# Kernel optimization log

Measured on AMD Instinct MI355X. Metric: run time of the kernel, lower is better.

## Reference

```python
import jax, jax.numpy as jnp
import numpy as np

N_DIM = 768
HIDDEN_DIM = 768
BATCH = 4
SEQ = 2048


def setup_inputs() -> dict:
    key = jax.random.key(0)
    ks = jax.random.split(key, 9)
    s_in = 1.0 / np.sqrt(N_DIM)
    s_h = 1.0 / np.sqrt(HIDDEN_DIM)
    return {
        "x": jax.random.normal(ks[0], (BATCH, SEQ, N_DIM), dtype=jnp.float32),
        # torch Linear weights: [out_features, in_features]
        "wq": jax.random.uniform(ks[1], (HIDDEN_DIM, N_DIM), jnp.float32, -s_in, s_in),
        "bq": jax.random.uniform(ks[2], (HIDDEN_DIM,), jnp.float32, -s_in, s_in),
        "wk": jax.random.uniform(ks[3], (HIDDEN_DIM, N_DIM), jnp.float32, -s_in, s_in),
        "bk": jax.random.uniform(ks[4], (HIDDEN_DIM,), jnp.float32, -s_in, s_in),
        "wv": jax.random.uniform(ks[5], (HIDDEN_DIM, N_DIM), jnp.float32, -s_in, s_in),
        "bv": jax.random.uniform(ks[6], (HIDDEN_DIM,), jnp.float32, -s_in, s_in),
        "wo": jax.random.uniform(ks[7], (N_DIM, HIDDEN_DIM), jnp.float32, -s_h, s_h),
        "bo": jax.random.uniform(ks[8], (N_DIM,), jnp.float32, -s_h, s_h),
    }


def reference(x, wq, bq, wk, bk, wv, bv, wo, bo):
    # q,k,v: [B, S, H]
    q = jnp.einsum("bsd,hd->bsh", x, wq) + bq
    k = jnp.einsum("bsd,hd->bsh", x, wk) + bk
    v = jnp.einsum("bsd,hd->bsh", x, wv) + bv
    # NOTE: faithful to source — no 1/sqrt(d) scaling, no mask.
    scores = jnp.einsum("bqh,bkh->bqk", q, k)  # [B, S, S]
    attn = jax.nn.softmax(scores, axis=-1)
    y = jnp.einsum("bqk,bkh->bqh", attn, v)  # [B, S, H]
    out = jnp.einsum("bsh,dh->bsd", y, wo) + bo
    return out
```

## Files before the change

kernel.cpp:

```cpp
#include <hip/hip_runtime.h>

typedef _Float16 f16;
typedef _Float16 f16x8 __attribute__((ext_vector_type(8)));
typedef float f32x4 __attribute__((ext_vector_type(4)));

#define GLD16(g, l) __builtin_amdgcn_global_load_lds( \
    (const __attribute__((address_space(1))) void*)(g), \
    (__attribute__((address_space(3))) void*)(l), 16, 0, 0)

template <typename OutT, int BM, int BN, int MODE, int MINW>
__global__ __launch_bounds__(256, MINW)
void gemm_kernel(const f16* __restrict__ A, long sA,
                 const f16* __restrict__ B, long sB,
                 void* __restrict__ Cv, long sC,
                 void* __restrict__ C2v,
                 const float* __restrict__ bias,
                 const float* __restrict__ bias2,
                 int N, int K)
{
    constexpr int FM = BM / 32;
    constexpr int FN = BN / 32;
    constexpr int IA = BM / 32;
    constexpr int IB = BN / 32;

    OutT* C  = (OutT*)Cv;
    OutT* C2 = (OutT*)C2v;
    const int tid  = threadIdx.x;
    const int wave = tid >> 6;
    const int lane = tid & 63;
    const int bz   = blockIdx.z;
    A += (long)bz * sA;
    B += (long)bz * sB;
    C += (long)bz * sC;
    const long bm = (long)blockIdx.x * BM;
    const long bn = (long)blockIdx.y * BN;

    __shared__ f16 sAt[BM * 64];
    __shared__ f16 sBt[BN * 64];

    const int srow = lane >> 3;
    const int gch  = ((lane & 7) ^ srow) * 8;

    const f16* gAb = A + (bm + wave * (BM / 4) + srow) * (long)K + gch;
    const f16* gBb = B + (bn + wave * (BN / 4) + srow) * (long)K + gch;

    const int wm = (wave >> 1) * (BM / 2);
    const int wn = (wave & 1) * (BN / 2);
    const int lr = lane & 15;
    const int qd = lane >> 4;
    const int swz0 = ((0 * 4 + qd) ^ (lr & 7)) * 8;
    const int swz1 = ((1 * 4 + qd) ^ (lr & 7)) * 8;

    f32x4 acc[FM][FN] = {};

    for (int k0 = 0; k0 < K; k0 += 64) {
        #pragma unroll
        for (int i = 0; i < IA; ++i)
            GLD16(gAb + k0 + (long)i * 8 * K, &sAt[(wave * (BM / 4) + i * 8) * 64]);
        #pragma unroll
        for (int i = 0; i < IB; ++i)
            GLD16(gBb + k0 + (long)i * 8 * K, &sBt[(wave * (BN / 4) + i * 8) * 64]);
        __syncthreads();

        #pragma unroll
        for (int h = 0; h < 2; ++h) {
            const int swz = h ? swz1 : swz0;
            f16x8 af[FM], bf[FN];
            #pragma unroll
            for (int t = 0; t < FM; ++t)
                af[t] = *(const f16x8*)&sAt[(wm + t * 16 + lr) * 64 + swz];
            #pragma unroll
            for (int t = 0; t < FN; ++t)
                bf[t] = *(const f16x8*)&sBt[(wn + t * 16 + lr) * 64 + swz];
            #pragma unroll
            for (int tm = 0; tm < FM; ++tm)
                #pragma unroll
                for (int tn = 0; tn < FN; ++tn)
                    acc[tm][tn] = __builtin_amdgcn_mfma_f32_16x16x32_f16(
                        af[tm], bf[tn], acc[tm][tn], 0, 0, 0);
        }
        __syncthreads();
    }

    #pragma unroll
    for (int tn = 0; tn < FN; ++tn) {
        const long col = bn + wn + tn * 16 + lr;
        OutT* dst = C;
        long cc = col, stride = N;
        float bc = 0.f;
        if (MODE == 1) bc = bias[col];
        if (MODE == 3) {
            stride = 768;
            if (col >= 768) { dst = C2; cc = col - 768; bc = bias2[cc]; }
            else            { bc = bias[cc]; }
        }
        #pragma unroll
        for (int tm = 0; tm < FM; ++tm) {
            #pragma unroll
            for (int r = 0; r < 4; ++r) {
                const long row = bm + wm + tm * 16 + qd * 4 + r;
                float v = acc[tm][tn][r] + bc;
                if (MODE == 2) v += bias[row];
                dst[row * stride + cc] = (OutT)v;
            }
        }
    }
}

template <typename OutT, int BM, int BN, int MODE, int MINW>
__global__ __launch_bounds__(256, MINW)
void gemm_pipe4(const f16* __restrict__ A, long sA,
                const f16* __restrict__ B, long sB,
                void* __restrict__ Cv, long sC,
                void* __restrict__ C2v,
                const float* __restrict__ bias,
                const float* __restrict__ bias2,
                int N, int K)
{
    constexpr int FM = BM / 32;
    constexpr int FN = BN / 32;
    constexpr int IA = BM / 32;
    constexpr int IB = BN / 32;

    OutT* C  = (OutT*)Cv;
    OutT* C2 = (OutT*)C2v;
    const int tid  = threadIdx.x;
    const int wave = tid >> 6;
    const int lane = tid & 63;
    const int bz   = blockIdx.z;
    A += (long)bz * sA;
    B += (long)bz * sB;
    C += (long)bz * sC;
    const long bm = (long)blockIdx.x * BM;
    const long bn = (long)blockIdx.y * BN;

    __shared__ f16 sAt[2][BM * 64];
    __shared__ f16 sBt[2][BN * 64];

    const int srow = lane >> 3;
    const int gch  = ((lane & 7) ^ srow) * 8;

    const f16* gAb = A + (bm + wave * (BM / 4) + srow) * (long)K + gch;
    const f16* gBb = B + (bn + wave * (BN / 4) + srow) * (long)K + gch;

    const int wm = (wave >> 1) * (BM / 2);
    const int wn = (wave & 1) * (BN / 2);
    const int lr = lane & 15;
    const int qd = lane >> 4;
    const int swz0 = ((0 * 4 + qd) ^ (lr & 7)) * 8;
    const int swz1 = ((1 * 4 + qd) ^ (lr & 7)) * 8;

    f32x4 acc[FM][FN] = {};

    #pragma unroll
    for (int i = 0; i < IA; ++i)
        GLD16(gAb + (long)i * 8 * K, &sAt[0][(wave * (BM / 4) + i * 8) * 64]);
    #pragma unroll
    for (int i = 0; i < IB; ++i)
        GLD16(gBb + (long)i * 8 * K, &sBt[0][(wave * (BN / 4) + i * 8) * 64]);

    const int nt = K / 64;
    for (int t = 0; t < nt; ++t) {
        const int cur = t & 1;
        if (t + 1 < nt) {
            const long off = (long)(t + 1) * 64;
            #pragma unroll
            for (int i = 0; i < IA; ++i)
                GLD16(gAb + off + (long)i * 8 * K, &sAt[cur ^ 1][(wave * (BM / 4) + i * 8) * 64]);
            #pragma unroll
            for (int i = 0; i < IB; ++i)
                GLD16(gBb + off + (long)i * 8 * K, &sBt[cur ^ 1][(wave * (BN / 4) + i * 8) * 64]);
            asm volatile("s_waitcnt vmcnt(%0)" :: "n"(IA + IB));
        } else {
            asm volatile("s_waitcnt vmcnt(0)");
        }
        __builtin_amdgcn_s_barrier();

        #pragma unroll
        for (int h = 0; h < 2; ++h) {
            const int swz = h ? swz1 : swz0;
            f16x8 af[FM], bf[FN];
            #pragma unroll
            for (int t2 = 0; t2 < FM; ++t2)
                af[t2] = *(const f16x8*)&sAt[cur][(wm + t2 * 16 + lr) * 64 + swz];
            #pragma unroll
            for (int t2 = 0; t2 < FN; ++t2)
                bf[t2] = *(const f16x8*)&sBt[cur][(wn + t2 * 16 + lr) * 64 + swz];
            __builtin_amdgcn_s_setprio(1);
            #pragma unroll
            for (int tm = 0; tm < FM; ++tm)
                #pragma unroll
                for (int tn = 0; tn < FN; ++tn)
                    acc[tm][tn] = __builtin_amdgcn_mfma_f32_16x16x32_f16(
                        af[tm], bf[tn], acc[tm][tn], 0, 0, 0);
            __builtin_amdgcn_s_setprio(0);
        }
        __builtin_amdgcn_s_barrier();
    }

    #pragma unroll
    for (int tn = 0; tn < FN; ++tn) {
        const long col = bn + wn + tn * 16 + lr;
        OutT* dst = C;
        long cc = col, stride = N;
        float bc = 0.f;
        if (MODE == 1) bc = bias[col];
        if (MODE == 3) {
            stride = 768;
            if (col >= 768) { dst = C2; cc = col - 768; bc = bias2[cc]; }
            else            { bc = bias[cc]; }
        }
        #pragma unroll
        for (int tm = 0; tm < FM; ++tm) {
            #pragma unroll
            for (int r = 0; r < 4; ++r) {
                const long row = bm + wm + tm * 16 + qd * 4 + r;
                float v = acc[tm][tn][r] + bc;
                if (MODE == 2) v += bias[row];
                dst[row * stride + cc] = (OutT)v;
            }
        }
    }
}

__global__ __launch_bounds__(512, 2)
void gemm_pipe(const f16* __restrict__ A, long sA,
               const f16* __restrict__ B, long sB,
               f16* __restrict__ C, long sC,
               int N, int K)
{
    const int tid  = threadIdx.x;
    const int wave = tid >> 6;
    const int lane = tid & 63;
    const int bz   = blockIdx.z;
    A += (long)bz * sA;
    B += (long)bz * sB;
    C += (long)bz * sC;
    const long bm = (long)blockIdx.x * 256;
    const long bn = (long)blockIdx.y * 256;

    __shared__ f16 sAt[2][256 * 64];
    __shared__ f16 sBt[2][256 * 64];

    const int srow = lane >> 3;
    const int gch  = ((lane & 7) ^ srow) * 8;
    const f16* gA = A + (bm + wave * 32 + srow) * (long)K + gch;
    const f16* gB = B + (bn + wave * 32 + srow) * (long)K + gch;

    const int wm = (wave >> 2) * 128;
    const int wn = (wave & 3) * 64;
    const int lr = lane & 15;
    const int qd = lane >> 4;
    const int swz0 = ((0 * 4 + qd) ^ (lr & 7)) * 8;
    const int swz1 = ((1 * 4 + qd) ^ (lr & 7)) * 8;

    f32x4 acc[8][4] = {};

    #pragma unroll
    for (int i = 0; i < 4; ++i)
        GLD16(gA + (long)i * 8 * K, &sAt[0][(wave * 32 + i * 8) * 64]);
    #pragma unroll
    for (int i = 0; i < 4; ++i)
        GLD16(gB + (long)i * 8 * K, &sBt[0][(wave * 32 + i * 8) * 64]);

    const int nt = K / 64;
    for (int t = 0; t < nt; ++t) {
        const int cur = t & 1;
        if (t + 1 < nt) {
            const long off = (long)(t + 1) * 64;
            #pragma unroll
            for (int i = 0; i < 4; ++i)
                GLD16(gA + off + (long)i * 8 * K, &sAt[cur ^ 1][(wave * 32 + i * 8) * 64]);
            #pragma unroll
            for (int i = 0; i < 4; ++i)
                GLD16(gB + off + (long)i * 8 * K, &sBt[cur ^ 1][(wave * 32 + i * 8) * 64]);
            asm volatile("s_waitcnt vmcnt(8)");
        } else {
            asm volatile("s_waitcnt vmcnt(0)");
        }
        __builtin_amdgcn_s_barrier();

        #pragma unroll
        for (int h = 0; h < 2; ++h) {
            const int swz = h ? swz1 : swz0;
            f16x8 bf[4];
            #pragma unroll
            for (int c = 0; c < 4; ++c)
                bf[c] = *(const f16x8*)&sBt[cur][(wn + c * 16 + lr) * 64 + swz];
            #pragma unroll
            for (int rh = 0; rh < 2; ++rh) {
                f16x8 af[4];
                #pragma unroll
                for (int m = 0; m < 4; ++m)
                    af[m] = *(const f16x8*)&sAt[cur][(wm + rh * 64 + m * 16 + lr) * 64 + swz];
                __builtin_amdgcn_s_setprio(1);
                #pragma unroll
                for (int m = 0; m < 4; ++m)
                    #pragma unroll
                    for (int c = 0; c < 4; ++c)
                        acc[rh * 4 + m][c] = __builtin_amdgcn_mfma_f32_16x16x32_f16(
                            af[m], bf[c], acc[rh * 4 + m][c], 0, 0, 0);
                __builtin_amdgcn_s_setprio(0);
            }
        }
        __builtin_amdgcn_s_barrier();
    }

    #pragma unroll
    for (int cf = 0; cf < 4; ++cf) {
        const long col = bn + wn + cf * 16 + lr;
        #pragma unroll
        for (int rf = 0; rf < 8; ++rf) {
            #pragma unroll
            for (int r = 0; r < 4; ++r) {
                const long row = bm + wm + rf * 16 + qd * 4 + r;
                C[row * (long)N + col] = (f16)acc[rf][cf][r];
            }
        }
    }
}

__global__ __launch_bounds__(256)
void softmax_kernel(f16* __restrict__ S)
{
    const long row = blockIdx.x;
    f16* p = S + row * 2048;
    const int tid  = threadIdx.x;
    const int wave = tid >> 6;
    const int lane = tid & 63;

    f16x8 x = *(const f16x8*)&p[tid * 8];
    float v[8];
    float m = -1e30f;
    #pragma unroll
    for (int j = 0; j < 8; ++j) { v[j] = (float)x[j]; m = fmaxf(m, v[j]); }
    #pragma unroll
    for (int off = 32; off > 0; off >>= 1) m = fmaxf(m, __shfl_down(m, off));

    __shared__ float rm[4], rs[4];
    if (lane == 0) rm[wave] = m;
    __syncthreads();
    m = fmaxf(fmaxf(rm[0], rm[1]), fmaxf(rm[2], rm[3]));

    float s = 0.f;
    #pragma unroll
    for (int j = 0; j < 8; ++j) { v[j] = __expf(v[j] - m); s += v[j]; }
    #pragma unroll
    for (int off = 32; off > 0; off >>= 1) s += __shfl_down(s, off);
    if (lane == 0) rs[wave] = s;
    __syncthreads();
    s = rs[0] + rs[1] + rs[2] + rs[3];
    const float inv = 1.0f / s;

    f16x8 y;
    #pragma unroll
    for (int j = 0; j < 8; ++j) y[j] = (f16)(v[j] * inv);
    *(f16x8*)&p[tid * 8] = y;
}

__global__ __launch_bounds__(256)
void cvt_all_kernel(const float* __restrict__ x,
                    const float* __restrict__ w0, const float* __restrict__ w1,
                    const float* __restrict__ w2, const float* __restrict__ w3,
                    f16* __restrict__ x16, f16* __restrict__ w16)
{
    const float* in; f16* out; long i;
    if (blockIdx.x < 3072) {
        in = x; out = x16;
        i = ((long)blockIdx.x * 256 + threadIdx.x) * 8;
    } else {
        const int wb  = blockIdx.x - 3072;
        const int sel = wb / 288;
        in  = (sel == 0) ? w0 : (sel == 1) ? w1 : (sel == 2) ? w2 : w3;
        out = w16 + (long)sel * 589824;
        i = ((long)(wb - sel * 288) * 256 + threadIdx.x) * 8;
    }
    float4 a = *(const float4*)(in + i);
    float4 b = *(const float4*)(in + i + 4);
    f16x8 o;
    o[0] = (f16)a.x; o[1] = (f16)a.y; o[2] = (f16)a.z; o[3] = (f16)a.w;
    o[4] = (f16)b.x; o[5] = (f16)b.y; o[6] = (f16)b.z; o[7] = (f16)b.w;
    *(f16x8*)&out[i] = o;
}

extern "C" void kernel_launch(void* const* d_in, const int* in_sizes, int n_in,
                              void* d_out, int out_size, void* d_ws, size_t ws_size,
                              hipStream_t stream)
{
    const float* x  = (const float*)d_in[0];
    const float* wq = (const float*)d_in[1];
    const float* bq = (const float*)d_in[2];
    const float* wk = (const float*)d_in[3];
    const float* bk = (const float*)d_in[4];
    const float* wv = (const float*)d_in[5];
    const float* bv = (const float*)d_in[6];
    const float* wo = (const float*)d_in[7];
    const float* bo = (const float*)d_in[8];

    char* ws = (char*)d_ws;
    f16* x16 = (f16*)(ws + 0);
    f16* w16 = (f16*)(ws + 12582912);
    f16* Q   = (f16*)(ws + 17301504);
    f16* Kb  = (f16*)(ws + 29884416);
    f16* VT  = (f16*)(ws + 42467328);
    f16* S   = (f16*)(ws + 55050240);
    f16* Y   = (f16*)(ws + 88604672);

    f16* wv16 = w16 + 2 * 589824;
    f16* wo16 = w16 + 3 * 589824;

    cvt_all_kernel<<<4224, 256, 0, stream>>>(x, wq, wk, wv, wo, x16, w16);

    gemm_kernel<f16, 128, 128, 3, 3><<<dim3(64, 12, 1), 256, 0, stream>>>(
        x16, 0, w16, 0, Q, 0, Kb, bq, bk, 1536, 768);
    gemm_pipe4<f16, 64, 128, 2, 4><<<dim3(12, 16, 4), 256, 0, stream>>>(
        wv16, 0, x16, (long)2048 * 768, VT, (long)768 * 2048, nullptr,
        bv, nullptr, 2048, 768);
    gemm_pipe<<<dim3(8, 8, 4), 512, 0, stream>>>(
        Q, (long)2048 * 768, Kb, (long)2048 * 768, S, (long)2048 * 2048,
        2048, 768);
    softmax_kernel<<<8192, 256, 0, stream>>>(S);
    gemm_pipe4<f16, 128, 64, 0, 4><<<dim3(16, 12, 4), 256, 0, stream>>>(
        S, (long)2048 * 2048, VT, (long)768 * 2048, Y, (long)2048 * 768,
        nullptr, nullptr, nullptr, 768, 2048);
    gemm_pipe4<float, 128, 64, 1, 4><<<dim3(64, 12, 1), 256, 0, stream>>>(
        Y, 0, wo16, 0, (float*)d_out, 0, nullptr, bo, nullptr, 768, 768);
}
```

Before: 230.2 us.

## Replace double-buffered K=64 GEMM pipelines with 4-stage K=32 ring buffers

The two pipelined GEMM kernels move from a two-slot LDS double buffer with 64-wide K tiles to a four-slot ring of 32-wide K tiles. Three tiles are prefetched ahead, and each iteration uses a single barrier, so global-to-LDS loads get more latency slack. The LDS swizzle is redone for the narrower 32-element rows. In exchange there are twice as many iterations and barriers, and each barrier round carries less MFMA work.

```diff
diff --git a/kernel.cpp b/kernel.cpp
--- a/kernel.cpp
+++ b/kernel.cpp
@@ -7,6 +7,10 @@
 #define GLD16(g, l) __builtin_amdgcn_global_load_lds( \
     (const __attribute__((address_space(1))) void*)(g), \
     (__attribute__((address_space(3))) void*)(l), 16, 0, 0)
+
+#define WAITV(n) asm volatile("s_waitcnt vmcnt(%0)" :: "n"(n) : "memory")
+#define BAR() do { __builtin_amdgcn_s_barrier(); \
+                   __builtin_amdgcn_sched_barrier(0); } while (0)
 
 template <typename OutT, int BM, int BN, int MODE, int MINW>
 __global__ __launch_bounds__(256, MINW)
@@ -109,7 +113,7 @@
 
 template <typename OutT, int BM, int BN, int MODE, int MINW>
 __global__ __launch_bounds__(256, MINW)
-void gemm_pipe4(const f16* __restrict__ A, long sA,
+void gemm_ring4(const f16* __restrict__ A, long sA,
                 const f16* __restrict__ B, long sB,
                 void* __restrict__ Cv, long sC,
                 void* __restrict__ C2v,
@@ -119,8 +123,9 @@
 {
     constexpr int FM = BM / 32;
     constexpr int FN = BN / 32;
-    constexpr int IA = BM / 32;
-    constexpr int IB = BN / 32;
+    constexpr int IA = BM / 64;
+    constexpr int IB = BN / 64;
+    constexpr int L  = IA + IB;
 
     OutT* C  = (OutT*)Cv;
     OutT* C2 = (OutT*)C2v;
@@ -134,11 +139,11 @@
     const long bm = (long)blockIdx.x * BM;
     const long bn = (long)blockIdx.y * BN;
 
-    __shared__ f16 sAt[2][BM * 64];
-    __shared__ f16 sBt[2][BN * 64];
-
-    const int srow = lane >> 3;
-    const int gch  = ((lane & 7) ^ srow) * 8;
+    __shared__ f16 shA[4][BM * 32];
+    __shared__ f16 shB[4][BN * 32];
+
+    const int srow = lane >> 2;
+    const int gch  = ((lane & 3) ^ ((lane >> 3) & 3)) * 8;
 
     const f16* gAb = A + (bm + wave * (BM / 4) + srow) * (long)K + gch;
     const f16* gBb = B + (bn + wave * (BN / 4) + srow) * (long)K + gch;
@@ -147,56 +152,52 @@
     const int wn = (wave & 1) * (BN / 2);
     const int lr = lane & 15;
     const int qd = lane >> 4;
-    const int swz0 = ((0 * 4 + qd) ^ (lr & 7)) * 8;
-    const int swz1 = ((1 * 4 + qd) ^ (lr & 7)) * 8;
+    const int rdo = (qd ^ ((lr >> 1) & 3)) * 8;
 
     f32x4 acc[FM][FN] = {};
 
-    #pragma unroll
-    for (int i = 0; i < IA; ++i)
-        GLD16(gAb + (long)i * 8 * K, &sAt[0][(wave * (BM / 4) + i * 8) * 64]);
-    #pragma unroll
-    for (int i = 0; i < IB; ++i)
-        GLD16(gBb + (long)i * 8 * K, &sBt[0][(wave * (BN / 4) + i * 8) * 64]);
-
-    const int nt = K / 64;
-    for (int t = 0; t < nt; ++t) {
-        const int cur = t & 1;
-        if (t + 1 < nt) {
-            const long off = (long)(t + 1) * 64;
-            #pragma unroll
-            for (int i = 0; i < IA; ++i)
-                GLD16(gAb + off + (long)i * 8 * K, &sAt[cur ^ 1][(wave * (BM / 4) + i * 8) * 64]);
-            #pragma unroll
-            for (int i = 0; i < IB; ++i)
-                GLD16(gBb + off + (long)i * 8 * K, &sBt[cur ^ 1][(wave * (BN / 4) + i * 8) * 64]);
-            asm volatile("s_waitcnt vmcnt(%0)" :: "n"(IA + IB));
-        } else {
-            asm volatile("s_waitcnt vmcnt(0)");
-        }
-        __builtin_amdgcn_s_barrier();
-
-        #pragma unroll
-        for (int h = 0; h < 2; ++h) {
-            const int swz = h ? swz1 : swz0;
-            f16x8 af[FM], bf[FN];
-            #pragma unroll
-            for (int t2 = 0; t2 < FM; ++t2)
-                af[t2] = *(const f16x8*)&sAt[cur][(wm + t2 * 16 + lr) * 64 + swz];
-            #pragma unroll
-            for (int t2 = 0; t2 < FN; ++t2)
-                bf[t2] = *(const f16x8*)&sBt[cur][(wn + t2 * 16 + lr) * 64 + swz];
-            __builtin_amdgcn_s_setprio(1);
-            #pragma unroll
-            for (int tm = 0; tm < FM; ++tm)
-                #pragma unroll
-                for (int tn = 0; tn < FN; ++tn)
-                    acc[tm][tn] = __builtin_amdgcn_mfma_f32_16x16x32_f16(
-                        af[tm], bf[tn], acc[tm][tn], 0, 0, 0);
-            __builtin_amdgcn_s_setprio(0);
-        }
-        __builtin_amdgcn_s_barrier();
-    }
+    auto issue = [&](int tt) {
+        const int s = tt & 3;
+        const long ko = (long)tt * 32;
+        #pragma unroll
+        for (int i = 0; i < IA; ++i)
+            GLD16(gAb + ko + (long)i * 16 * K, &shA[s][(wave * (BM / 4) + i * 16) * 32]);
+        #pragma unroll
+        for (int i = 0; i < IB; ++i)
+            GLD16(gBb + ko + (long)i * 16 * K, &shB[s][(wave * (BN / 4) + i * 16) * 32]);
+    };
+
+    auto comp = [&](int tt) {
+        const int cur = tt & 3;
+        f16x8 af[FM], bf[FN];
+        #pragma unroll
+        for (int m = 0; m < FM; ++m)
+            af[m] = *(const f16x8*)&shA[cur][(wm + m * 16 + lr) * 32 + rdo];
+        #pragma unroll
+        for (int n = 0; n < FN; ++n)
+            bf[n] = *(const f16x8*)&shB[cur][(wn + n * 16 + lr) * 32 + rdo];
+        __builtin_amdgcn_s_setprio(1);
+        #pragma unroll
+        for (int m = 0; m < FM; ++m)
+            #pragma unroll
+            for (int n = 0; n < FN; ++n)
+                acc[m][n] = __builtin_amdgcn_mfma_f32_16x16x32_f16(
+                    af[m], bf[n], acc[m][n], 0, 0, 0);
+        __builtin_amdgcn_s_setprio(0);
+    };
+
+    const int nt = K / 32;
+    issue(0); issue(1); issue(2);
+
+    for (int t = 0; t < nt - 3; ++t) {
+        WAITV(2 * L);
+        BAR();
+        issue(t + 3);
+        comp(t);
+    }
+    WAITV(2 * L); BAR(); comp(nt - 3);
+    WAITV(L);     BAR(); comp(nt - 2);
+    WAITV(0);     BAR(); comp(nt - 1);
 
     #pragma unroll
     for (int tn = 0; tn < FN; ++tn) {
@@ -224,11 +225,12 @@
 }
 
 __global__ __launch_bounds__(512, 2)
-void gemm_pipe(const f16* __restrict__ A, long sA,
-               const f16* __restrict__ B, long sB,
-               f16* __restrict__ C, long sC,
-               int N, int K)
-{
+void gemm_ring8(const f16* __restrict__ A, long sA,
+                const f16* __restrict__ B, long sB,
+                f16* __restrict__ C, long sC,
+                int N, int K)
+{
+    constexpr int L = 4;
     const int tid  = threadIdx.x;
     const int wave = tid >> 6;
     const int lane = tid & 63;
@@ -239,11 +241,11 @@
     const long bm = (long)blockIdx.x * 256;
     const long bn = (long)blockIdx.y * 256;
 
-    __shared__ f16 sAt[2][256 * 64];
-    __shared__ f16 sBt[2][256 * 64];
-
-    const int srow = lane >> 3;
-    const int gch  = ((lane & 7) ^ srow) * 8;
+    __shared__ f16 shA[4][256 * 32];
+    __shared__ f16 shB[4][256 * 32];
+
+    const int srow = lane >> 2;
+    const int gch  = ((lane & 3) ^ ((lane >> 3) & 3)) * 8;
     const f16* gA = A + (bm + wave * 32 + srow) * (long)K + gch;
     const f16* gB = B + (bn + wave * 32 + srow) * (long)K + gch;
 
@@ -251,60 +253,56 @@
     const int wn = (wave & 3) * 64;
     const int lr = lane & 15;
     const int qd = lane >> 4;
-    const int swz0 = ((0 * 4 + qd) ^ (lr & 7)) * 8;
-    const int swz1 = ((1 * 4 + qd) ^ (lr & 7)) * 8;
+    const int rdo = (qd ^ ((lr >> 1) & 3)) * 8;
 
     f32x4 acc[8][4] = {};
 
-    #pragma unroll
-    for (int i = 0; i < 4; ++i)
-        GLD16(gA + (long)i * 8 * K, &sAt[0][(wave * 32 + i * 8) * 64]);
-    #pragma unroll
-    for (int i = 0; i < 4; ++i)
-        GLD16(gB + (long)i * 8 * K, &sBt[0][(wave * 32 + i * 8) * 64]);
-
-    const int nt = K / 64;
-    for (int t = 0; t < nt; ++t) {
-        const int cur = t & 1;
-        if (t + 1 < nt) {
-            const long off = (long)(t + 1) * 64;
-            #pragma unroll
-            for (int i = 0; i < 4; ++i)
-                GLD16(gA + off + (long)i * 8 * K, &sAt[cur ^ 1][(wave * 32 + i * 8) * 64]);
-            #pragma unroll
-            for (int i = 0; i < 4; ++i)
-                GLD16(gB + off + (long)i * 8 * K, &sBt[cur ^ 1][(wave * 32 + i * 8) * 64]);
-            asm volatile("s_waitcnt vmcnt(8)");
-        } else {
-            asm volatile("s_waitcnt vmcnt(0)");
-        }
-        __builtin_amdgcn_s_barrier();
-
-        #pragma unroll
-        for (int h = 0; h < 2; ++h) {
-            const int swz = h ? swz1 : swz0;
-            f16x8 bf[4];
-            #pragma unroll
-            for (int c = 0; c < 4; ++c)
-                bf[c] = *(const f16x8*)&sBt[cur][(wn + c * 16 + lr) * 64 + swz];
-            #pragma unroll
-            for (int rh = 0; rh < 2; ++rh) {
-                f16x8 af[4];
+    auto issue = [&](int tt) {
+        const int s = tt & 3;
+        const long ko = (long)tt * 32;
+        #pragma unroll
+        for (int i = 0; i < 2; ++i)
+            GLD16(gA + ko + (long)i * 16 * K, &shA[s][(wave * 32 + i * 16) * 32]);
+        #pragma unroll
+        for (int i = 0; i < 2; ++i)
+            GLD16(gB + ko + (long)i * 16 * K, &shB[s][(wave * 32 + i * 16) * 32]);
+    };
+
+    auto comp = [&](int tt) {
+        const int cur = tt & 3;
+        f16x8 bf[4];
+        #pragma unroll
+        for (int n = 0; n < 4; ++n)
+            bf[n] = *(const f16x8*)&shB[cur][(wn + n * 16 + lr) * 32 + rdo];
+        #pragma unroll
+        for (int rh = 0; rh < 2; ++rh) {
+            f16x8 af[4];
+            #pragma unroll
+            for (int m = 0; m < 4; ++m)
+                af[m] = *(const f16x8*)&shA[cur][(wm + rh * 64 + m * 16 + lr) * 32 + rdo];
+            __builtin_amdgcn_s_setprio(1);
+            #pragma unroll
+            for (int m = 0; m < 4; ++m)
                 #pragma unroll
-                for (int m = 0; m < 4; ++m)
-                    af[m] = *(const f16x8*)&sAt[cur][(wm + rh * 64 + m * 16 + lr) * 64 + swz];
-                __builtin_amdgcn_s_setprio(1);
-                #pragma unroll
-                for (int m = 0; m < 4; ++m)
-                    #pragma unroll
-                    for (int c = 0; c < 4; ++c)
-                        acc[rh * 4 + m][c] = __builtin_amdgcn_mfma_f32_16x16x32_f16(
-                            af[m], bf[c], acc[rh * 4 + m][c], 0, 0, 0);
-                __builtin_amdgcn_s_setprio(0);
-            }
-        }
-        __builtin_amdgcn_s_barrier();
-    }
+                for (int n = 0; n < 4; ++n)
+                    acc[rh * 4 + m][n] = __builtin_amdgcn_mfma_f32_16x16x32_f16(
+                        af[m], bf[n], acc[rh * 4 + m][n], 0, 0, 0);
+            __builtin_amdgcn_s_setprio(0);
+        }
+    };
+
+    const int nt = K / 32;
+    issue(0); issue(1); issue(2);
+
+    for (int t = 0; t < nt - 3; ++t) {
+        WAITV(2 * L);
+        BAR();
+        issue(t + 3);
+        comp(t);
+    }
+    WAITV(2 * L); BAR(); comp(nt - 3);
+    WAITV(L);     BAR(); comp(nt - 2);
+    WAITV(0);     BAR(); comp(nt - 1);
 
     #pragma unroll
     for (int cf = 0; cf < 4; ++cf) {
@@ -413,16 +411,16 @@
 
     gemm_kernel<f16, 128, 128, 3, 3><<<dim3(64, 12, 1), 256, 0, stream>>>(
         x16, 0, w16, 0, Q, 0, Kb, bq, bk, 1536, 768);
-    gemm_pipe4<f16, 64, 128, 2, 4><<<dim3(12, 16, 4), 256, 0, stream>>>(
+    gemm_ring4<f16, 64, 128, 2, 4><<<dim3(12, 16, 4), 256, 0, stream>>>(
         wv16, 0, x16, (long)2048 * 768, VT, (long)768 * 2048, nullptr,
         bv, nullptr, 2048, 768);
-    gemm_pipe<<<dim3(8, 8, 4), 512, 0, stream>>>(
+    gemm_ring8<<<dim3(8, 8, 4), 512, 0, stream>>>(
         Q, (long)2048 * 768, Kb, (long)2048 * 768, S, (long)2048 * 2048,
         2048, 768);
     softmax_kernel<<<8192, 256, 0, stream>>>(S);
-    gemm_pipe4<f16, 128, 64, 0, 4><<<dim3(16, 12, 4), 256, 0, stream>>>(
+    gemm_ring4<f16, 128, 64, 0, 4><<<dim3(16, 12, 4), 256, 0, stream>>>(
         S, (long)2048 * 2048, VT, (long)768 * 2048, Y, (long)2048 * 768,
         nullptr, nullptr, nullptr, 768, 2048);
-    gemm_pipe4<float, 128, 64, 1, 4><<<dim3(64, 12, 1), 256, 0, stream>>>(
+    gemm_ring4<float, 128, 64, 1, 4><<<dim3(64, 12, 1), 256, 0, stream>>>(
         Y, 0, wo16, 0, (float*)d_out, 0, nullptr, bo, nullptr, 768, 768);
 }
```

Measured after the change: 260.4 us. 1.13x slower.
